# Kernel optimization log

Hardware: AMD Instinct MI355X
Metric: run time of the kernel (lower is better)

## Reference

```python
import jax, jax.numpy as jnp
import numpy as np

T, B, E, H = 256, 8, 512, 32
EXP = 512            # number of expanded (periodic-image) keys
SMOOTH = 20.0        # smooth_factor


def setup_inputs() -> dict:
    key = jax.random.key(0)
    ks = jax.random.split(key, 12)
    s = 1.0 / np.sqrt(E)
    return {
        "query": jax.random.normal(ks[0], (T, B, E), dtype=jnp.float32),
        "outcell_index": jax.random.randint(ks[1], (B, EXP), 0, T),
        "expand_mask": jax.random.bernoulli(ks[2], 0.1, (B, EXP)),
        "key_padding_mask": jax.random.bernoulli(ks[3], 0.1, (B, T)),
        "local_attention_weight": jax.random.uniform(ks[4], (B, T, T + EXP), dtype=jnp.float32),
        "Wq": jax.random.normal(ks[5], (E, E), dtype=jnp.float32) * s,
        "bq": jnp.zeros((E,), dtype=jnp.float32),
        "Wk": jax.random.normal(ks[6], (E, E), dtype=jnp.float32) * s,   # k_bias=False
        "Wv": jax.random.normal(ks[7], (E, E), dtype=jnp.float32) * s,
        "bv": jnp.zeros((E,), dtype=jnp.float32),
        "Wo": jax.random.normal(ks[8], (E, E), dtype=jnp.float32) * s,
        "bo": jnp.zeros((E,), dtype=jnp.float32),
    }


def reference(query, outcell_index, expand_mask, key_padding_mask,
              local_attention_weight, Wq, bq, Wk, Wv, bv, Wo, bo):
    t, b, e = query.shape
    hd = e // H
    # QKV projections (torch Linear: y = x @ W.T + b)
    q = jnp.einsum('tbe,fe->tbf', query, Wq) + bq
    k = jnp.einsum('tbe,fe->tbf', query, Wk)          # no k bias
    v = jnp.einsum('tbe,fe->tbf', query, Wv) + bv
    # PBC gather-expand K/V along the time axis
    oc = outcell_index.T[:, :, None]                  # [EXP, B, 1]
    k = jnp.concatenate([k, jnp.take_along_axis(k, oc, axis=0)], axis=0)  # [S,B,E]
    v = jnp.concatenate([v, jnp.take_along_axis(v, oc, axis=0)], axis=0)
    s_len = k.shape[0]
    # [len, B, E] -> [B, H, len, hd]
    qh = q.reshape(t, b, H, hd).transpose(1, 2, 0, 3)
    kh = k.reshape(s_len, b, H, hd).transpose(1, 2, 0, 3)
    vh = v.reshape(s_len, b, H, hd).transpose(1, 2, 0, 3)
    # NOTE: forward() never applies self.scaling in this path (faithful)
    scores = jnp.einsum('bhtd,bhsd->bhts', qh, kh)    # [B,H,T,S]
    law = local_attention_weight[:, None]             # [B,1,T,S]
    scores = (scores + SMOOTH) * law - SMOOTH         # smooth softmax
    kpm = jnp.concatenate([key_padding_mask, expand_mask], axis=1)  # [B,S]
    scores = jnp.where(kpm[:, None, None, :], -jnp.inf, scores)
    probs = jax.nn.softmax(scores, axis=-1)
    probs = probs * law                               # post-softmax reweight
    attn = jnp.einsum('bhts,bhsd->bhtd', probs, vh)   # [B,H,T,hd]
    attn = attn.transpose(2, 0, 1, 3).reshape(t, b, e)
    return jnp.einsum('tbe,fe->tbf', attn, Wo) + bo
```

## Files before the change

### kernel.cpp

```cpp
#include <hip/hip_runtime.h>
#include <stdint.h>

#define T_ 256
#define B_ 8
#define E_ 512
#define H_ 32
#define HD_ 16
#define EXP_ 512
#define S_ 768
#define M_ 2048
#define SMOOTH_ 20.0f
#define PSTR 40
#define VSTR 800
#define OSTR 20
#define LOG2E_ 1.44269504f
#define MB0_  (-100.988655f)

typedef __attribute__((ext_vector_type(8)))  short bf16x8;
typedef __attribute__((ext_vector_type(4)))  float f32x4;
typedef __attribute__((ext_vector_type(16))) float f32x16;

__device__ __forceinline__ unsigned int pku(float a, float b)
{
    return ((__float_as_uint(a) + 0x8000u) >> 16) |
           ((__float_as_uint(b) + 0x8000u) & 0xFFFF0000u);
}
__device__ __forceinline__ ushort bf1(float a)
{
    unsigned int u = __float_as_uint(a);
    u = u + 0x7FFFu + ((u >> 16) & 1u);
    return (ushort)(u >> 16);
}

union U16 { uint4 u; bf16x8 v; };

__global__ __launch_bounds__(1024, 4)
void qkv_attn_kernel(const float* __restrict__ X,
                     const float* __restrict__ Wq, const float* __restrict__ Wk,
                     const float* __restrict__ Wv,
                     const float* __restrict__ bq, const float* __restrict__ bv,
                     const float* __restrict__ LAW,
                     const int* __restrict__ kpm, const int* __restrict__ em,
                     const int* __restrict__ oc, ushort* __restrict__ Ab)
{
    __shared__ __align__(16) char raw[102400];
    ushort* Ks  = (ushort*)(raw);
    ushort* Vt  = (ushort*)(raw + 24576);
    ushort* Qi  = (ushort*)(raw + 50176);
    float*  msf = (float*) (raw + 58368);
    ushort* Pbb = (ushort*)(raw + 61440);
    ushort* As  = (ushort*)(raw);
    ushort* Bs  = (ushort*)(raw + 36864);
    float*  Obuf= (float*) (raw);
    float*  Zb  = (float*) (raw + 58368);
    ushort* Ob  = Qi;

    const int bh  = blockIdx.x;
    const int b   = bh >> 5;
    const int h   = bh & 31;
    const int tid = threadIdx.x;
    const int w   = tid >> 6;
    const int l   = tid & 63;

    const int r0 = tid >> 3;
    const int c8 = tid & 7;
    const float* Xc0 = &X[((size_t)r0 * 8 + b) * E_ + c8 * 8];
    const float* Xc1 = Xc0 + (size_t)128 * 8 * E_;

    const int wr = tid >> 3;
    const bool wload = (tid < 384);
    const float* Wsel = (wr < 16) ? Wq : (wr < 32 ? Wk : Wv);
    const float* Wr = &Wsel[((size_t)(h * 16 + (wr & 15))) * E_ + c8 * 8];
    ushort* Bxw = &Bs[wr * 72 + c8 * 8];

    f32x4 acc[3];
#pragma unroll
    for (int m = 0; m < 3; ++m) acc[m] = (f32x4){0.f, 0.f, 0.f, 0.f};

    float4 xa0, xa1, xb0, xb1, wp0, wp1;
    xa0 = *(const float4*)&Xc0[0]; xa1 = *(const float4*)&Xc0[4];
    xb0 = *(const float4*)&Xc1[0]; xb1 = *(const float4*)&Xc1[4];
    if (wload) { wp0 = *(const float4*)&Wr[0]; wp1 = *(const float4*)&Wr[4]; }

    const int ln = l & 15;
    const int lg = l >> 4;

    for (int it = 0; it < 8; ++it) {
        __syncthreads();
        *(uint4*)&As[r0 * 72 + c8 * 8] =
            make_uint4(pku(xa0.x, xa0.y), pku(xa0.z, xa0.w),
                       pku(xa1.x, xa1.y), pku(xa1.z, xa1.w));
        *(uint4*)&As[(r0 + 128) * 72 + c8 * 8] =
            make_uint4(pku(xb0.x, xb0.y), pku(xb0.z, xb0.w),
                       pku(xb1.x, xb1.y), pku(xb1.z, xb1.w));
        if (wload)
            *(uint4*)&Bxw[0] = make_uint4(pku(wp0.x, wp0.y), pku(wp0.z, wp0.w),
                                          pku(wp1.x, wp1.y), pku(wp1.z, wp1.w));
        __syncthreads();
        if (it < 7) {
            Xc0 += 64; Xc1 += 64;
            xa0 = *(const float4*)&Xc0[0]; xa1 = *(const float4*)&Xc0[4];
            xb0 = *(const float4*)&Xc1[0]; xb1 = *(const float4*)&Xc1[4];
            if (wload) { Wr += 64; wp0 = *(const float4*)&Wr[0]; wp1 = *(const float4*)&Wr[4]; }
        }
#pragma unroll
        for (int kb = 0; kb < 2; ++kb) {
            bf16x8 af = *(const bf16x8*)&As[(w * 16 + ln) * 72 + kb * 32 + lg * 8];
#pragma unroll
            for (int m = 0; m < 3; ++m) {
                bf16x8 bfm = *(const bf16x8*)&Bs[(m * 16 + ln) * 72 + kb * 32 + lg * 8];
                acc[m] = __builtin_amdgcn_mfma_f32_16x16x32_bf16(af, bfm, acc[m], 0, 0, 0);
            }
        }
    }

    __syncthreads();

    {
        const float bqv = bq[h * 16 + ln];
        const float bvv = bv[h * 16 + ln];
#pragma unroll
        for (int r = 0; r < 4; ++r) {
            const int t = w * 16 + lg * 4 + r;
            Qi[t * 16 + ln]   = bf1(acc[0][r] + bqv);
            Ks[t * 16 + ln]   = bf1(acc[1][r]);
            Vt[ln * VSTR + t] = bf1(acc[2][r] + bvv);
        }
    }
    __syncthreads();

    if (tid < 512) {
        const int j   = tid;
        const int src = oc[b * EXP_ + j];
        uint4 k0 = *(const uint4*)&Ks[src * 16];
        uint4 k1 = *(const uint4*)&Ks[src * 16 + 8];
        *(uint4*)&Ks[(T_ + j) * 16]     = k0;
        *(uint4*)&Ks[(T_ + j) * 16 + 8] = k1;
    } else {
        const int j   = tid - 512;
        const int src = oc[b * EXP_ + j];
#pragma unroll
        for (int d = 0; d < 16; ++d)
            Vt[d * VSTR + T_ + j] = Vt[d * VSTR + src];
    }
    if (tid < 768) {
        const int s = tid;
        const int m = (s < T_) ? kpm[b * T_ + s] : em[b * EXP_ + (s - T_)];
        msf[s] = m ? -1.0e5f : MB0_;
    }
    __syncthreads();

    const int slane = l & 31;
    const int khalf = l >> 5;
    const int tl = l & 15;
    const int kg = l >> 4;
    const int tq = w & 7;
    const int sh = w >> 3;

    bf16x8 qf = *(const bf16x8*)&Qi[(tq * 32 + slane) * 16 + khalf * 8];

    const f32x16 zero16 = {0.f,0.f,0.f,0.f,0.f,0.f,0.f,0.f,
                           0.f,0.f,0.f,0.f,0.f,0.f,0.f,0.f};
    f32x4 o0 = {0.f, 0.f, 0.f, 0.f};
    f32x4 o1 = {0.f, 0.f, 0.f, 0.f};
    float zacc[16];
#pragma unroll
    for (int r = 0; r < 16; ++r) zacc[r] = 0.f;

    const float* lawb = &LAW[((size_t)b * T_ + tq * 32 + khalf * 4) * S_ + slane];
    ushort* pw = &Pbb[w * 32 * PSTR + slane];
    ushort* pt = &Pbb[w * 32 * PSTR];

    for (int i = sh * 12; i < sh * 12 + 12; ++i) {
        bf16x8 kf = *(const bf16x8*)&Ks[(i * 32 + slane) * 16 + khalf * 8];

        float lw[16];
        const float* lp = lawb + i * 32;
#pragma unroll
        for (int r = 0; r < 16; ++r)
            lw[r] = lp[(size_t)((r & 3) + 8 * (r >> 2)) * S_];

        f32x16 sc = __builtin_amdgcn_mfma_f32_32x32x16_bf16(qf, kf, zero16, 0, 0, 0);
        const float mb = msf[i * 32 + slane];

#pragma unroll
        for (int r = 0; r < 16; ++r) {
            const float lwK = lw[r] * LOG2E_;
            const float arg = __builtin_fmaf(sc[r], lwK,
                              __builtin_fmaf(lwK, SMOOTH_, mb));
            const float e = __builtin_amdgcn_exp2f(arg);
            zacc[r] += e;
            const float p = e * lw[r];
            pw[((r & 3) + 8 * (r >> 2) + 4 * khalf) * PSTR] =
                (ushort)((__float_as_uint(p) + 0x8000u) >> 16);
        }

        bf16x8 vf = *(const bf16x8*)&Vt[tl * VSTR + i * 32 + kg * 8];
        {
            const ushort* pr0 = &pt[(0 * 16 + tl) * PSTR + kg * 8];
            U16 u;
            uint2 a0 = *(const uint2*)pr0;
            uint2 a1 = *(const uint2*)(pr0 + 4);
            u.u = make_uint4(a0.x, a0.y, a1.x, a1.y);
            o0 = __builtin_amdgcn_mfma_f32_16x16x32_bf16(vf, u.v, o0, 0, 0, 0);
            const ushort* pr1 = &pt[(1 * 16 + tl) * PSTR + kg * 8];
            uint2 b0 = *(const uint2*)pr1;
            uint2 b1 = *(const uint2*)(pr1 + 4);
            u.u = make_uint4(b0.x, b0.y, b1.x, b1.y);
            o1 = __builtin_amdgcn_mfma_f32_16x16x32_bf16(vf, u.v, o1, 0, 0, 0);
        }
    }

#pragma unroll
    for (int m = 1; m < 32; m <<= 1) {
#pragma unroll
        for (int r = 0; r < 16; ++r)
            zacc[r] += __shfl_xor(zacc[r], m);
    }

    __syncthreads();

    if (l == 0 || l == 32) {
#pragma unroll
        for (int r = 0; r < 16; ++r)
            Zb[sh * 256 + tq * 32 + (r & 3) + 8 * (r >> 2) + 4 * khalf] = zacc[r];
    }
    if (sh == 1) {
#pragma unroll
        for (int th = 0; th < 2; ++th) {
            const f32x4 o = th ? o1 : o0;
            *(float4*)&Obuf[((size_t)(tq * 32 + th * 16 + tl)) * OSTR + kg * 4] =
                make_float4(o[0], o[1], o[2], o[3]);
        }
    }
    __syncthreads();

    if (sh == 0) {
#pragma unroll
        for (int th = 0; th < 2; ++th) {
            const int t = tq * 32 + th * 16 + tl;
            const float Zt  = Zb[t] + Zb[256 + t];
            const float inv = (Zt > 0.f) ? 1.f / Zt : 0.f;
            float4 po = *(const float4*)&Obuf[(size_t)t * OSTR + kg * 4];
            const f32x4 o = th ? o1 : o0;
            float ov[4] = {(o[0] + po.x) * inv, (o[1] + po.y) * inv,
                           (o[2] + po.z) * inv, (o[3] + po.w) * inv};
            *(uint*)&Ob[t * 16 + kg * 4]     = pku(ov[0], ov[1]);
            *(uint*)&Ob[t * 16 + kg * 4 + 2] = pku(ov[2], ov[3]);
        }
    }
    __syncthreads();

    {
        const int t  = tid >> 2;
        const int q4 = tid & 3;
        *(uint2*)&Ab[((size_t)(t * 8 + b)) * E_ + h * 16 + q4 * 4] =
            *(const uint2*)&Ob[t * 16 + q4 * 4];
    }
}

__device__ __forceinline__ void out_gemm_body(const ushort* __restrict__ Xh,
                                              const float* __restrict__ Wf,
                                              f32x4 acc[2][2],
                                              ushort* As, ushort* Bs)
{
    const int tid  = threadIdx.x;
    const int lrow = tid >> 2;
    const int kq   = tid & 3;
    const int l    = tid & 63;
    const int w    = tid >> 6;
    const int wm   = w & 1;
    const int wn   = w >> 1;
    const int lq   = l >> 4;
    const int ln   = l & 15;

    ushort* Aw = &As[lrow * 72 + kq * 16];
    ushort* Bw = &Bs[lrow * 72 + kq * 16];

    uint4  ha0 = *(const uint4*)&Xh[0];
    uint4  ha1 = *(const uint4*)&Xh[8];
    float4 fb0 = *(const float4*)&Wf[0];
    float4 fb1 = *(const float4*)&Wf[4];
    float4 fb2 = *(const float4*)&Wf[8];
    float4 fb3 = *(const float4*)&Wf[12];

    for (int it = 0; it < E_ / 64; ++it) {
        __syncthreads();
        *(uint4*)&Aw[0] = ha0;
        *(uint4*)&Aw[8] = ha1;
        *(uint4*)&Bw[0] = make_uint4(pku(fb0.x, fb0.y), pku(fb0.z, fb0.w),
                                     pku(fb1.x, fb1.y), pku(fb1.z, fb1.w));
        *(uint4*)&Bw[8] = make_uint4(pku(fb2.x, fb2.y), pku(fb2.z, fb2.w),
                                     pku(fb3.x, fb3.y), pku(fb3.z, fb3.w));
        __syncthreads();
        if (it < E_ / 64 - 1) {
            Xh += 64;
            ha0 = *(const uint4*)&Xh[0];
            ha1 = *(const uint4*)&Xh[8];
            Wf += 64;
            fb0 = *(const float4*)&Wf[0];
            fb1 = *(const float4*)&Wf[4];
            fb2 = *(const float4*)&Wf[8];
            fb3 = *(const float4*)&Wf[12];
        }
#pragma unroll
        for (int kb = 0; kb < 2; ++kb) {
            bf16x8 af0 = *(const bf16x8*)&As[(32 * wm + ln) * 72 + 32 * kb + lq * 8];
            bf16x8 af1 = *(const bf16x8*)&As[(32 * wm + 16 + ln) * 72 + 32 * kb + lq * 8];
            bf16x8 bf0 = *(const bf16x8*)&Bs[(32 * wn + ln) * 72 + 32 * kb + lq * 8];
            bf16x8 bf1 = *(const bf16x8*)&Bs[(32 * wn + 16 + ln) * 72 + 32 * kb + lq * 8];
            acc[0][0] = __builtin_amdgcn_mfma_f32_16x16x32_bf16(af0, bf0, acc[0][0], 0, 0, 0);
            acc[0][1] = __builtin_amdgcn_mfma_f32_16x16x32_bf16(af0, bf1, acc[0][1], 0, 0, 0);
            acc[1][0] = __builtin_amdgcn_mfma_f32_16x16x32_bf16(af1, bf0, acc[1][0], 0, 0, 0);
            acc[1][1] = __builtin_amdgcn_mfma_f32_16x16x32_bf16(af1, bf1, acc[1][1], 0, 0, 0);
        }
    }
}

__global__ __launch_bounds__(256)
void out_gemm(const ushort* __restrict__ Ab, const float* __restrict__ Wo,
              const float* __restrict__ bo, float* __restrict__ dst)
{
    __shared__ __align__(16) ushort AsBs[2 * 64 * 72];
    ushort* As = AsBs;
    ushort* Bs = AsBs + 64 * 72;

    const int m0 = blockIdx.y * 64;
    const int n0 = blockIdx.x * 64;

    f32x4 acc[2][2];
#pragma unroll
    for (int i = 0; i < 2; ++i)
#pragma unroll
        for (int j = 0; j < 2; ++j)
            acc[i][j] = (f32x4){0.f, 0.f, 0.f, 0.f};

    const int tid  = threadIdx.x;
    const int lrow = tid >> 2;
    const int kq   = tid & 3;
    out_gemm_body(&Ab[(size_t)(m0 + lrow) * E_ + kq * 16],
                  &Wo[(size_t)(n0 + lrow) * E_ + kq * 16],
                  acc, As, Bs);

    const int l  = tid & 63;
    const int w  = tid >> 6;
    const int wm = w & 1;
    const int wn = w >> 1;
    const int lq = l >> 4;
    const int ln = l & 15;

    const float bo0 = bo[n0 + 32 * wn + ln];
    const float bo1 = bo[n0 + 32 * wn + 16 + ln];

    __syncthreads();
    float* Lf = (float*)AsBs;
#pragma unroll
    for (int j = 0; j < 2; ++j) {
        const float bb = j ? bo1 : bo0;
#pragma unroll
        for (int i = 0; i < 2; ++i)
#pragma unroll
            for (int r = 0; r < 4; ++r)
                Lf[(32 * wm + 16 * i + lq * 4 + r) * 68 + 32 * wn + 16 * j + ln] =
                    acc[i][j][r] + bb;
    }
    __syncthreads();

    {
        const int lm = tid & 63;
        const int hh = tid >> 6;
        float* dp = &dst[(size_t)(m0 + lm) * E_ + n0 + hh * 16];
#pragma unroll
        for (int c = 0; c < 4; ++c) {
            float4 v = *(const float4*)&Lf[lm * 68 + hh * 16 + c * 4];
            *(float4*)&dp[c * 4] = v;
        }
    }
}

extern "C" void kernel_launch(void* const* d_in, const int* in_sizes, int n_in,
                              void* d_out, int out_size, void* d_ws, size_t ws_size,
                              hipStream_t stream)
{
    const float* query = (const float*)d_in[0];
    const int*   oc    = (const int*)d_in[1];
    const int*   em    = (const int*)d_in[2];
    const int*   kpm   = (const int*)d_in[3];
    const float* law   = (const float*)d_in[4];
    const float* Wq    = (const float*)d_in[5];
    const float* bq    = (const float*)d_in[6];
    const float* Wk    = (const float*)d_in[7];
    const float* Wv    = (const float*)d_in[8];
    const float* bv    = (const float*)d_in[9];
    const float* Wo    = (const float*)d_in[10];
    const float* bo    = (const float*)d_in[11];
    float* out = (float*)d_out;

    ushort* Ab = (ushort*)d_ws;

    qkv_attn_kernel<<<B_ * H_, 1024, 0, stream>>>(query, Wq, Wk, Wv, bq, bv,
                                                  law, kpm, em, oc, Ab);

    dim3 go(E_ / 64, M_ / 64, 1);
    out_gemm<<<go, 256, 0, stream>>>(Ab, Wo, bo, out);
}
```

Before: 124.2 us.

## Retile output GEMM to 32x64 tiles with K=128 steps and remap block-to-batch/head

The output projection GEMM moves from 64x64 tiles with 64-wide K steps to 32x64 tiles with 128-wide K steps. That doubles the grid to 512 blocks and halves the number of barrier-separated iterations, and the launch bounds now request two blocks per CU. The attention kernel's block index mapping is also changed so consecutive blocks go to different batches of the same head, which changes L2 locality for weight and query reads. In exchange, the smaller M tile re-reads and re-converts more of Wo overall, and each thread holds more register staging.

```diff
diff --git a/kernel.cpp b/kernel.cpp
--- a/kernel.cpp
+++ b/kernel.cpp
@@ -56,8 +56,8 @@
     ushort* Ob  = Qi;
 
     const int bh  = blockIdx.x;
-    const int b   = bh >> 5;
-    const int h   = bh & 31;
+    const int b   = bh & 7;
+    const int h   = bh >> 3;
     const int tid = threadIdx.x;
     const int w   = tid >> 6;
     const int l   = tid & 63;
@@ -259,88 +259,40 @@
     }
 }
 
-__device__ __forceinline__ void out_gemm_body(const ushort* __restrict__ Xh,
-                                              const float* __restrict__ Wf,
-                                              f32x4 acc[2][2],
-                                              ushort* As, ushort* Bs)
-{
-    const int tid  = threadIdx.x;
-    const int lrow = tid >> 2;
-    const int kq   = tid & 3;
-    const int l    = tid & 63;
-    const int w    = tid >> 6;
-    const int wm   = w & 1;
-    const int wn   = w >> 1;
-    const int lq   = l >> 4;
-    const int ln   = l & 15;
-
-    ushort* Aw = &As[lrow * 72 + kq * 16];
-    ushort* Bw = &Bs[lrow * 72 + kq * 16];
-
-    uint4  ha0 = *(const uint4*)&Xh[0];
-    uint4  ha1 = *(const uint4*)&Xh[8];
-    float4 fb0 = *(const float4*)&Wf[0];
-    float4 fb1 = *(const float4*)&Wf[4];
-    float4 fb2 = *(const float4*)&Wf[8];
-    float4 fb3 = *(const float4*)&Wf[12];
-
-    for (int it = 0; it < E_ / 64; ++it) {
-        __syncthreads();
-        *(uint4*)&Aw[0] = ha0;
-        *(uint4*)&Aw[8] = ha1;
-        *(uint4*)&Bw[0] = make_uint4(pku(fb0.x, fb0.y), pku(fb0.z, fb0.w),
-                                     pku(fb1.x, fb1.y), pku(fb1.z, fb1.w));
-        *(uint4*)&Bw[8] = make_uint4(pku(fb2.x, fb2.y), pku(fb2.z, fb2.w),
-                                     pku(fb3.x, fb3.y), pku(fb3.z, fb3.w));
-        __syncthreads();
-        if (it < E_ / 64 - 1) {
-            Xh += 64;
-            ha0 = *(const uint4*)&Xh[0];
-            ha1 = *(const uint4*)&Xh[8];
-            Wf += 64;
-            fb0 = *(const float4*)&Wf[0];
-            fb1 = *(const float4*)&Wf[4];
-            fb2 = *(const float4*)&Wf[8];
-            fb3 = *(const float4*)&Wf[12];
-        }
-#pragma unroll
-        for (int kb = 0; kb < 2; ++kb) {
-            bf16x8 af0 = *(const bf16x8*)&As[(32 * wm + ln) * 72 + 32 * kb + lq * 8];
-            bf16x8 af1 = *(const bf16x8*)&As[(32 * wm + 16 + ln) * 72 + 32 * kb + lq * 8];
-            bf16x8 bf0 = *(const bf16x8*)&Bs[(32 * wn + ln) * 72 + 32 * kb + lq * 8];
-            bf16x8 bf1 = *(const bf16x8*)&Bs[(32 * wn + 16 + ln) * 72 + 32 * kb + lq * 8];
-            acc[0][0] = __builtin_amdgcn_mfma_f32_16x16x32_bf16(af0, bf0, acc[0][0], 0, 0, 0);
-            acc[0][1] = __builtin_amdgcn_mfma_f32_16x16x32_bf16(af0, bf1, acc[0][1], 0, 0, 0);
-            acc[1][0] = __builtin_amdgcn_mfma_f32_16x16x32_bf16(af1, bf0, acc[1][0], 0, 0, 0);
-            acc[1][1] = __builtin_amdgcn_mfma_f32_16x16x32_bf16(af1, bf1, acc[1][1], 0, 0, 0);
-        }
-    }
-}
-
-__global__ __launch_bounds__(256)
+__global__ __launch_bounds__(256, 2)
 void out_gemm(const ushort* __restrict__ Ab, const float* __restrict__ Wo,
               const float* __restrict__ bo, float* __restrict__ dst)
 {
-    __shared__ __align__(16) ushort AsBs[2 * 64 * 72];
-    ushort* As = AsBs;
-    ushort* Bs = AsBs + 64 * 72;
-
-    const int m0 = blockIdx.y * 64;
+    __shared__ __align__(16) ushort sbuf[96 * 136];
+    ushort* As = sbuf;
+    ushort* Bs = sbuf + 32 * 136;
+
     const int n0 = blockIdx.x * 64;
-
-    f32x4 acc[2][2];
-#pragma unroll
-    for (int i = 0; i < 2; ++i)
-#pragma unroll
-        for (int j = 0; j < 2; ++j)
-            acc[i][j] = (f32x4){0.f, 0.f, 0.f, 0.f};
-
-    const int tid  = threadIdx.x;
-    const int lrow = tid >> 2;
-    const int kq   = tid & 3;
-    out_gemm_body(&Ab[(size_t)(m0 + lrow) * E_ + kq * 16],
-                  &Wo[(size_t)(n0 + lrow) * E_ + kq * 16],
-                  acc, As, Bs);
+    const int m0 = blockIdx.y * 32;
+
+    const int tid = threadIdx.x;
+    const int arow = tid >> 3;
+    const int acol = (tid & 7) * 16;
+    const int brow = tid >> 2;
+    const int bcol = (tid & 3) * 32;
+
+    const ushort* Ap = &Ab[(size_t)(m0 + arow) * E_ + acol];
+    const float*  Wp = &Wo[(size_t)(n0 + brow) * E_ + bcol];
+
+    f32x4 acc[2];
+    acc[0] = (f32x4){0.f, 0.f, 0.f, 0.f};
+    acc[1] = (f32x4){0.f, 0.f, 0.f, 0.f};
+
+    uint4  ha0 = *(const uint4*)&Ap[0];
+    uint4  ha1 = *(const uint4*)&Ap[8];
+    float4 f0 = *(const float4*)&Wp[0];
+    float4 f1 = *(const float4*)&Wp[4];
+    float4 f2 = *(const float4*)&Wp[8];
+    float4 f3 = *(const float4*)&Wp[12];
+    float4 f4 = *(const float4*)&Wp[16];
+    float4 f5 = *(const float4*)&Wp[20];
+    float4 f6 = *(const float4*)&Wp[24];
+    float4 f7 = *(const float4*)&Wp[28];
 
     const int l  = tid & 63;
     const int w  = tid >> 6;
@@ -349,32 +301,65 @@
     const int lq = l >> 4;
     const int ln = l & 15;
 
-    const float bo0 = bo[n0 + 32 * wn + ln];
-    const float bo1 = bo[n0 + 32 * wn + 16 + ln];
-
-    __syncthreads();
-    float* Lf = (float*)AsBs;
+    for (int it = 0; it < 4; ++it) {
+        __syncthreads();
+        *(uint4*)&As[arow * 136 + acol]     = ha0;
+        *(uint4*)&As[arow * 136 + acol + 8] = ha1;
+        *(uint4*)&Bs[brow * 136 + bcol]      = make_uint4(pku(f0.x, f0.y), pku(f0.z, f0.w),
+                                                          pku(f1.x, f1.y), pku(f1.z, f1.w));
+        *(uint4*)&Bs[brow * 136 + bcol + 8]  = make_uint4(pku(f2.x, f2.y), pku(f2.z, f2.w),
+                                                          pku(f3.x, f3.y), pku(f3.z, f3.w));
+        *(uint4*)&Bs[brow * 136 + bcol + 16] = make_uint4(pku(f4.x, f4.y), pku(f4.z, f4.w),
+                                                          pku(f5.x, f5.y), pku(f5.z, f5.w));
+        *(uint4*)&Bs[brow * 136 + bcol + 24] = make_uint4(pku(f6.x, f6.y), pku(f6.z, f6.w),
+                                                          pku(f7.x, f7.y), pku(f7.z, f7.w));
+        __syncthreads();
+        if (it < 3) {
+            Ap += 128; Wp += 128;
+            ha0 = *(const uint4*)&Ap[0];
+            ha1 = *(const uint4*)&Ap[8];
+            f0 = *(const float4*)&Wp[0];
+            f1 = *(const float4*)&Wp[4];
+            f2 = *(const float4*)&Wp[8];
+            f3 = *(const float4*)&Wp[12];
+            f4 = *(const float4*)&Wp[16];
+            f5 = *(const float4*)&Wp[20];
+            f6 = *(const float4*)&Wp[24];
+            f7 = *(const float4*)&Wp[28];
+        }
+#pragma unroll
+        for (int kb = 0; kb < 4; ++kb) {
+            bf16x8 af  = *(const bf16x8*)&As[(wm * 16 + ln) * 136 + kb * 32 + lq * 8];
+            bf16x8 bv0 = *(const bf16x8*)&Bs[(wn * 32 + ln) * 136 + kb * 32 + lq * 8];
+            bf16x8 bv1 = *(const bf16x8*)&Bs[(wn * 32 + 16 + ln) * 136 + kb * 32 + lq * 8];
+            acc[0] = __builtin_amdgcn_mfma_f32_16x16x32_bf16(af, bv0, acc[0], 0, 0, 0);
+            acc[1] = __builtin_amdgcn_mfma_f32_16x16x32_bf16(af, bv1, acc[1], 0, 0, 0);
+        }
+    }
+
+    const float bo0 = bo[n0 + wn * 32 + ln];
+    const float bo1 = bo[n0 + wn * 32 + 16 + ln];
+
+    __syncthreads();
+    float* Lf = (float*)sbuf;
 #pragma unroll
     for (int j = 0; j < 2; ++j) {
         const float bb = j ? bo1 : bo0;
-#pragma unroll
-        for (int i = 0; i < 2; ++i)
-#pragma unroll
-            for (int r = 0; r < 4; ++r)
-                Lf[(32 * wm + 16 * i + lq * 4 + r) * 68 + 32 * wn + 16 * j + ln] =
-                    acc[i][j][r] + bb;
+        const f32x4 a = acc[j];
+#pragma unroll
+        for (int r = 0; r < 4; ++r)
+            Lf[(wm * 16 + lq * 4 + r) * 68 + wn * 32 + j * 16 + ln] = a[r] + bb;
     }
     __syncthreads();
 
     {
-        const int lm = tid & 63;
-        const int hh = tid >> 6;
-        float* dp = &dst[(size_t)(m0 + lm) * E_ + n0 + hh * 16];
-#pragma unroll
-        for (int c = 0; c < 4; ++c) {
-            float4 v = *(const float4*)&Lf[lm * 68 + hh * 16 + c * 4];
-            *(float4*)&dp[c * 4] = v;
-        }
+        const int orow = tid >> 3;
+        const int oc8  = (tid & 7) * 8;
+        float* dp = &dst[(size_t)(m0 + orow) * E_ + n0 + oc8];
+        float4 v0 = *(const float4*)&Lf[orow * 68 + oc8];
+        float4 v1 = *(const float4*)&Lf[orow * 68 + oc8 + 4];
+        *(float4*)&dp[0] = v0;
+        *(float4*)&dp[4] = v1;
     }
 }
 
@@ -401,6 +386,6 @@
     qkv_attn_kernel<<<B_ * H_, 1024, 0, stream>>>(query, Wq, Wk, Wv, bq, bv,
                                                   law, kpm, em, oc, Ab);
 
-    dim3 go(E_ / 64, M_ / 64, 1);
+    dim3 go(E_ / 64, M_ / 32, 1);
     out_gemm<<<go, 256, 0, stream>>>(Ab, Wo, bo, out);
 }
```

After: 125.2 us. About the same (+0.7%).
